# Performance work log

Hardware: AMD Instinct MI355X
Metric: run time of the kernel (lower is better)

## Reference

```python
import jax, jax.numpy as jnp
import numpy as np

NUM, B, C, H, W = 2, 8, 512, 32, 32


def setup_inputs() -> dict:
    key = jax.random.key(0)
    ks = jax.random.split(key, 6)
    s = 0.02  # weight init scale
    return {
        "feat_sources": jax.random.normal(ks[0], (NUM, B, C, H, W), jnp.float32),
        "feat_targets": jax.random.normal(ks[1], (NUM, B, C, H, W), jnp.float32),
        # 1x1 conv == per-pixel channel matmul: weight [num, C_out, C_in], bias [num, C]
        "Wq": jax.random.normal(ks[2], (NUM, C, C), jnp.float32) * s,
        "bq": jnp.zeros((NUM, C), jnp.float32),
        "Wk": jax.random.normal(ks[3], (NUM, C, C), jnp.float32) * s,
        "bk": jnp.zeros((NUM, C), jnp.float32),
        "Wv": jax.random.normal(ks[4], (NUM, C, C), jnp.float32) * s,
        "bv": jnp.zeros((NUM, C), jnp.float32),
    }


def reference(feat_sources, feat_targets, Wq, bq, Wk, bk, Wv, bv):
    num, Bt, Ct, Ht, Wt = feat_targets.shape
    HW = Ht * Wt
    tgt = feat_targets.reshape(num, Bt, Ct, HW)  # queries/values come from targets
    src = feat_sources.reshape(num, Bt, Ct, HW)  # keys come from sources

    # 1x1 conv projections (batched over the `num` heads of convs)
    Q = jnp.einsum('ioc,ibcn->ibno', Wq, tgt) + bq[:, None, None, :]   # (num, B, HW, C)
    K = jnp.einsum('joc,jbcn->jbon', Wk, src) + bk[:, None, :, None]   # (num, B, C, HW)
    V = jnp.einsum('ioc,ibcn->ibon', Wv, tgt) + bv[:, None, :, None]   # (num, B, C, HW)

    # energy[i, j] = bmm(pro_query_i, pro_key_j) over all target/source pairs
    energy = jnp.einsum('ibnc,jbcm->ijbnm', Q, K)                      # (num, num, B, HW, HW)

    # alpha: softmax over sources j of the scalar mean energy per (i, j)
    means = energy.mean(axis=(2, 3, 4))                                # (num, num)
    alphas = jax.nn.softmax(means, axis=1)

    # per-source softmax over keys, then summed across sources (torch.stack(...).sum(0))
    attn = jax.nn.softmax(energy, axis=-1).sum(axis=1)                 # (num, B, HW, HW)

    # out[b, c, n] = sum_m V[b, c, m] * attn[b, n, m]  (bmm(value, attention^T))
    out = jnp.einsum('ibcm,ibnm->ibcn', V, attn).reshape(num, Bt, Ct, Ht, Wt)
    return out, alphas
```

## Files before the change

kernel.cpp:

```cpp
#include <hip/hip_runtime.h>

#define NUMH 2
#define BATCH 8
#define CCH 512
#define HWN 1024

typedef unsigned short u16;
typedef unsigned int u32;
typedef _Float16 f16;
typedef __attribute__((ext_vector_type(8))) _Float16 f16x8;
typedef __attribute__((ext_vector_type(8))) short bf16x8;
typedef __attribute__((ext_vector_type(4))) float f32x4;

__device__ __forceinline__ u16 f2h(float x) {
    union { f16 h; u16 u; } cv;
    cv.h = (f16)x;
    return cv.u;
}
__device__ __forceinline__ u16 f2bf(float x) {
    u32 u = __float_as_uint(x);
    return (u16)((u + 0x7fffu + ((u >> 16) & 1u)) >> 16);
}

__device__ __forceinline__ float waveReduceSum(float v) {
#pragma unroll
    for (int off = 32; off > 0; off >>= 1) v += __shfl_xor(v, off);
    return v;
}

__device__ __forceinline__ void swz_decode(int& x, int& y, int& z) {
    const int gx = gridDim.x, gy = gridDim.y;
    const int nwg = gx * gy * gridDim.z;
    const int fid = blockIdx.x + gx * (blockIdx.y + gy * blockIdx.z);
    const int cpx = nwg >> 3;
    int swz = (fid & 7) * cpx + (fid >> 3);
    x = swz % gx; swz /= gx;
    y = swz % gy; z = swz / gy;
}

__global__ void zero_means_kernel(float* means) {
    if (threadIdx.x < 4) means[threadIdx.x] = 0.0f;
}

__global__ __launch_bounds__(256) void reduce_rs_kernel(const float* __restrict__ rs,
                                                        float* __restrict__ ls, int n) {
    const int idx = blockIdx.x * 256 + threadIdx.x;
    if (idx >= n) return;
    const int slice = idx >> 10, col = idx & 1023;
    const float* p = rs + ((size_t)slice * 16) * HWN + col;
    float s = 0.0f;
#pragma unroll
    for (int k = 0; k < 16; k++) s += p[k * HWN];
    ls[idx] = s;
}

__device__ __forceinline__ void stage_tile(const u16* __restrict__ src, int ld, int k0,
                                           u16* lds_arr, int w, int l) {
#pragma unroll
    for (int inst = 0; inst < 2; inst++) {
        const int p = w * 128 + inst * 64 + l;
        const int n = p >> 2;
        const int k4 = (p & 3) ^ ((n >> 1) & 3);
        const u16* g = src + n * ld + k0 + k4 * 8;
        u16* lp = lds_arr + (w * 128 + inst * 64) * 8;
        __builtin_amdgcn_global_load_lds(
            (const __attribute__((address_space(1))) u32*)g,
            (__attribute__((address_space(3))) u32*)lp, 16, 0, 0);
    }
}

template<bool BF>
__device__ __forceinline__ void mfma_block(const u16* sA, const u16* sB,
                                           int wr, int wc, int fr, int kq, f32x4 acc[4][4]) {
#define SLOT(row) (((row) * 4 + ((kq) ^ (((row) >> 1) & 3))) * 8)
    if constexpr (BF) {
        bf16x8 a[4], b[4];
#pragma unroll
        for (int mi = 0; mi < 4; mi++) a[mi] = *(const bf16x8*)(sA + SLOT(wr * 64 + mi * 16 + fr));
#pragma unroll
        for (int ni = 0; ni < 4; ni++) b[ni] = *(const bf16x8*)(sB + SLOT(wc * 64 + ni * 16 + fr));
#pragma unroll
        for (int mi = 0; mi < 4; mi++)
#pragma unroll
            for (int ni = 0; ni < 4; ni++)
                acc[mi][ni] = __builtin_amdgcn_mfma_f32_16x16x32_bf16(a[mi], b[ni], acc[mi][ni], 0, 0, 0);
    } else {
        f16x8 a[4], b[4];
#pragma unroll
        for (int mi = 0; mi < 4; mi++) a[mi] = *(const f16x8*)(sA + SLOT(wr * 64 + mi * 16 + fr));
#pragma unroll
        for (int ni = 0; ni < 4; ni++) b[ni] = *(const f16x8*)(sB + SLOT(wc * 64 + ni * 16 + fr));
#pragma unroll
        for (int mi = 0; mi < 4; mi++)
#pragma unroll
            for (int ni = 0; ni < 4; ni++)
                acc[mi][ni] = __builtin_amdgcn_mfma_f32_16x16x32_f16(a[mi], b[ni], acc[mi][ni], 0, 0, 0);
    }
#undef SLOT
}

template<bool BF>
__device__ __forceinline__ void mm_core(const u16* __restrict__ A, const u16* __restrict__ B,
                                        int K, int ldA, int ldB, u16* s, f32x4 acc[4][4]) {
    const int t = threadIdx.x, w = t >> 6, l = t & 63;
    const int wr = w >> 1, wc = w & 1, fr = l & 15, kq = l >> 4;
    u16 *sA0 = s, *sA1 = s + 4096, *sB0 = s + 8192, *sB1 = s + 12288;
    for (int k0 = 0; k0 < K; k0 += 64) {
        __syncthreads();
        stage_tile(A, ldA, k0, sA0, w, l);
        stage_tile(A, ldA, k0 + 32, sA1, w, l);
        stage_tile(B, ldB, k0, sB0, w, l);
        stage_tile(B, ldB, k0 + 32, sB1, w, l);
        __syncthreads();
        mfma_block<BF>(sA0, sB0, wr, wc, fr, kq, acc);
        mfma_block<BF>(sA1, sB1, wr, wc, fr, kq, acc);
    }
}

#define ACC_INIT(acc)                                         \
    f32x4 acc[4][4];                                          \
    _Pragma("unroll") for (int mi_ = 0; mi_ < 4; mi_++)       \
    _Pragma("unroll") for (int ni_ = 0; ni_ < 4; ni_++)       \
        acc[mi_][ni_] = (f32x4){0.f, 0.f, 0.f, 0.f};

#define SMEM_BYTES 32768

template<bool BF, bool BCOL, bool BROW>
__device__ __forceinline__ void epi_h16(char* smem, const f32x4 acc[4][4],
                                        const float* biasCol, const float* biasRow,
                                        u16* O, int ldO) {
    const int t = threadIdx.x, w = t >> 6, l = t & 63;
    const int wr = w >> 1, wc = w & 1, fr = l & 15, fq = l >> 4;
    u16* sb16 = (u16*)smem;
    u32* sb32 = (u32*)smem;
#pragma unroll
    for (int half = 0; half < 2; half++) {
        __syncthreads();
        if (wr == half) {
#pragma unroll
            for (int ni = 0; ni < 4; ni++) {
                const int col = wc * 64 + ni * 16 + fr;
                const float bc = BCOL ? biasCol[col] : 0.0f;
#pragma unroll
                for (int mi = 0; mi < 4; mi++)
#pragma unroll
                    for (int r = 0; r < 4; r++) {
                        const int lrow = mi * 16 + fq * 4 + r;
                        const float v = acc[mi][ni][r] + bc +
                                        (BROW ? biasRow[half * 64 + lrow] : 0.0f);
                        sb16[lrow * 132 + col] = BF ? f2bf(v) : f2h(v);
                    }
            }
        }
        __syncthreads();
#pragma unroll
        for (int it = 0; it < 4; it++) {
            const int idx = it * 256 + t;
            const int rr = idx >> 4, ch = idx & 15;
            const uint4 v4 = *(const uint4*)&sb32[rr * 66 + ch * 4];
            *(uint4*)&O[(size_t)(half * 64 + rr) * ldO + ch * 8] = v4;
        }
    }
}

template<bool SCALE>
__device__ __forceinline__ void epi_f32(char* smem, const f32x4 acc[4][4],
                                        const float* ls, float* O, int ldO) {
    const int t = threadIdx.x, w = t >> 6, l = t & 63;
    const int wr = w >> 1, wc = w & 1, fr = l & 15, fq = l >> 4;
    float* sf = (float*)smem;
#pragma unroll
    for (int q = 0; q < 4; q++) {
        __syncthreads();
        if (wr == (q >> 1)) {
            const int mi0 = (q & 1) * 2;
#pragma unroll
            for (int ni = 0; ni < 4; ni++) {
                const int col = wc * 64 + ni * 16 + fr;
                const float inv = SCALE ? 1.0f / ls[col] : 1.0f;
#pragma unroll
                for (int mm = 0; mm < 2; mm++)
#pragma unroll
                    for (int r = 0; r < 4; r++) {
                        const int lrow = mm * 16 + fq * 4 + r;
                        sf[lrow * 132 + col] = acc[mi0 + mm][ni][r] * inv;
                    }
            }
        }
        __syncthreads();
#pragma unroll
        for (int it = 0; it < 4; it++) {
            const int idx = it * 256 + t;
            const int rr = idx >> 5, ch = idx & 31;
            const float4 v4 = *(const float4*)&sf[rr * 132 + ch * 4];
            *(float4*)&O[(size_t)(q * 32 + rr) * ldO + ch * 4] = v4;
        }
    }
}

__global__ __launch_bounds__(256) void tconv_kernel(
    const float* __restrict__ tgt, const float* __restrict__ src,
    u16* __restrict__ Tt, u16* __restrict__ St) {
    __shared__ float s[64][65];
    const int z = blockIdx.z;
    const int ib = z & 15;
    const float* X = (z >> 4 ? src : tgt) + (size_t)ib * CCH * HWN;
    u16* O = (z >> 4 ? St : Tt) + (size_t)ib * HWN * CCH;
    const int n0 = blockIdx.x * 64, c0 = blockIdx.y * 64;
    const int t = threadIdx.x;
    {
        const int cc = t >> 4, nch = (t & 15) * 4;
#pragma unroll
        for (int r = 0; r < 4; r++) {
            const float4 v = *(const float4*)&X[(size_t)(c0 + cc + r * 16) * HWN + n0 + nch];
            s[cc + r * 16][nch + 0] = v.x;
            s[cc + r * 16][nch + 1] = v.y;
            s[cc + r * 16][nch + 2] = v.z;
            s[cc + r * 16][nch + 3] = v.w;
        }
    }
    __syncthreads();
    const int nl = t >> 2;
    const int cb = (t & 3) * 16;
    __attribute__((aligned(16))) u16 hbuf[16];
#pragma unroll
    for (int cc = 0; cc < 16; cc++) hbuf[cc] = f2h(s[cb + cc][nl]);
    const size_t orow = (size_t)(n0 + nl) * CCH + c0 + cb;
    *(uint4*)&O[orow + 0] = *(const uint4*)&hbuf[0];
    *(uint4*)&O[orow + 8] = *(const uint4*)&hbuf[8];
}

__global__ __launch_bounds__(256) void convw_kernel(
    const float* __restrict__ Wq, const float* __restrict__ Wk, const float* __restrict__ Wv,
    u16* __restrict__ Wqh, u16* __restrict__ Wkh, u16* __restrict__ Wvh) {
    const int idx = (blockIdx.x * 256 + threadIdx.x) * 4;
    {
        const float4 v = *(const float4*)&Wq[idx];
        uint2 h = {(u32)f2h(v.x) | ((u32)f2h(v.y) << 16), (u32)f2h(v.z) | ((u32)f2h(v.w) << 16)};
        *(uint2*)&Wqh[idx] = h;
    }
    {
        const float4 v = *(const float4*)&Wk[idx];
        uint2 h = {(u32)f2h(v.x) | ((u32)f2h(v.y) << 16), (u32)f2h(v.z) | ((u32)f2h(v.w) << 16)};
        *(uint2*)&Wkh[idx] = h;
    }
    {
        const float4 v = *(const float4*)&Wv[idx];
        uint2 h = {(u32)f2h(v.x) | ((u32)f2h(v.y) << 16), (u32)f2h(v.z) | ((u32)f2h(v.w) << 16)};
        *(uint2*)&Wvh[idx] = h;
    }
}

__global__ __launch_bounds__(256) void proj_qk_kernel(
    const u16* __restrict__ Tt, const u16* __restrict__ St,
    const u16* __restrict__ Wqh, const u16* __restrict__ Wkh,
    const float* __restrict__ bq, const float* __restrict__ bk,
    u16* __restrict__ Qp, u16* __restrict__ Kp) {
    __shared__ __align__(16) char smem[SMEM_BYTES];
    int bx, by, z;
    swz_decode(bx, by, z);
    const int b = z & 7, i = (z >> 3) & 1, p = z >> 4;
    const size_t ib = (size_t)(i * BATCH + b) * HWN * CCH;
    const u16* A = (p ? St : Tt) + ib;
    const u16* B = (p ? Wkh : Wqh) + (size_t)i * CCH * CCH;
    const float* bias = (p ? bk : bq) + i * CCH;
    u16* O = (p ? Kp : Qp) + ib;
    const int tile_m = by * 128, tile_n = bx * 128;

    ACC_INIT(acc)
    mm_core<false>(A + (size_t)tile_m * CCH, B + (size_t)tile_n * CCH,
                   CCH, CCH, CCH, (u16*)smem, acc);

    epi_h16<false, true, false>(smem, acc, bias + tile_n, nullptr,
                                O + (size_t)tile_m * CCH + tile_n, CCH);
}

__global__ __launch_bounds__(256) void proj_v_kernel(
    const u16* __restrict__ Wvh, const u16* __restrict__ Tt,
    const float* __restrict__ bvv, u16* __restrict__ Vb) {
    __shared__ __align__(16) char smem[SMEM_BYTES];
    int bx, by, z;
    swz_decode(bx, by, z);
    const int b = z & 7, i = z >> 3;
    const size_t ib = (size_t)(i * BATCH + b) * HWN * CCH;
    const u16* A = Wvh + (size_t)i * CCH * CCH;
    const u16* B = Tt + ib;
    const int tile_m = by * 128, tile_n = bx * 128;

    ACC_INIT(acc)
    mm_core<false>(A + (size_t)tile_m * CCH, B + (size_t)tile_n * CCH,
                   CCH, CCH, CCH, (u16*)smem, acc);

    u16* Ov = Vb + (size_t)(i * BATCH + b) * CCH * HWN;
    epi_h16<true, false, true>(smem, acc, nullptr, bvv + i * CCH + tile_m,
                               Ov + (size_t)tile_m * HWN + tile_n, HWN);
}

__global__ __launch_bounds__(256) void gemmE_kernel(
    const u16* __restrict__ Qp, const u16* __restrict__ Kp,
    u16* __restrict__ P, float* __restrict__ rs, float* __restrict__ means,
    int b0, int Bc) {
    __shared__ __align__(16) char smem[33792];
    __shared__ float redsum[4];
    int bx, by, z;
    swz_decode(bx, by, z);
    const int j = z & 1, ib2 = z >> 1;
    const int i = ib2 / Bc, bb = ib2 % Bc, b = b0 + bb;
    const size_t offA = (size_t)(i * BATCH + b) * HWN * CCH;
    const size_t offB = (size_t)(j * BATCH + b) * HWN * CCH;
    const int tile_m = by * 128, tile_n = bx * 128;
    u16* Po = P + (size_t)(ib2 * 2 + j) * HWN * HWN + (size_t)tile_m * HWN + tile_n;

    ACC_INIT(acc)
    mm_core<false>(Qp + offA + (size_t)tile_m * CCH, Kp + offB + (size_t)tile_n * CCH,
                   CCH, CCH, CCH, (u16*)smem, acc);

    const int t = threadIdx.x, w = t >> 6, l = t & 63;
    const int wr = w >> 1, wc = w & 1, fr = l & 15, fq = l >> 4;
    u16* sb16 = (u16*)smem;
    u32* sb32 = (u32*)smem;
    float* rsp = rs + ((size_t)(ib2 * 2 + j) * 16 + (bx * 2 + wc)) * HWN;
    __syncthreads();
    float tsum = 0.0f;
    float rowacc[4][4];
#pragma unroll
    for (int mi = 0; mi < 4; mi++)
#pragma unroll
        for (int r = 0; r < 4; r++) rowacc[mi][r] = 0.0f;
#pragma unroll
    for (int ni = 0; ni < 4; ni++) {
        const int col = wc * 64 + ni * 16 + fr;
#pragma unroll
        for (int mi = 0; mi < 4; mi++)
#pragma unroll
            for (int r = 0; r < 4; r++) {
                const int row = wr * 64 + mi * 16 + fq * 4 + r;
                const float raw = acc[mi][ni][r];
                tsum += raw;
                const float ex = __expf(raw);
                rowacc[mi][r] += ex;
                sb16[row * 132 + col] = f2bf(ex);
            }
    }
    tsum = waveReduceSum(tsum);
    if (l == 0) redsum[w] = tsum;
#pragma unroll
    for (int mi = 0; mi < 4; mi++)
#pragma unroll
        for (int r = 0; r < 4; r++) {
            float v = rowacc[mi][r];
            v += __shfl_xor(v, 1); v += __shfl_xor(v, 2);
            v += __shfl_xor(v, 4); v += __shfl_xor(v, 8);
            if (fr == 0) rsp[tile_m + wr * 64 + mi * 16 + fq * 4 + r] = v;
        }
    __syncthreads();
    if (t == 0) atomicAdd(&means[i * 2 + j], redsum[0] + redsum[1] + redsum[2] + redsum[3]);
#pragma unroll
    for (int it = 0; it < 8; it++) {
        const int idx = it * 256 + t;
        const int rr = idx >> 4, ch = idx & 15;
        const uint4 v4 = *(const uint4*)&sb32[rr * 66 + ch * 4];
        *(uint4*)&Po[(size_t)rr * HWN + ch * 8] = v4;
    }
}

__global__ __launch_bounds__(256) void gemmOut_kernel(
    const u16* __restrict__ Vb, const u16* __restrict__ P, const float* __restrict__ ls,
    float* __restrict__ outp, int b0, int Bc) {
    __shared__ __align__(16) char smem[SMEM_BYTES];
    int bx, by, ib2;
    swz_decode(bx, by, ib2);
    const int i = ib2 / Bc, bb = ib2 % Bc, b = b0 + bb;
    const u16* A = Vb + (size_t)(i * BATCH + b) * CCH * HWN;
    const u16* P0 = P + (size_t)(ib2 * 2 + 0) * HWN * HWN;
    const u16* P1 = P + (size_t)(ib2 * 2 + 1) * HWN * HWN;
    const float* ls0 = ls + (size_t)(ib2 * 2 + 0) * HWN;
    const float* ls1 = ls + (size_t)(ib2 * 2 + 1) * HWN;
    float* O = outp + (size_t)(i * BATCH + b) * CCH * HWN;
    const int tile_m = by * 128, tile_n = bx * 128;
    const int t = threadIdx.x, w = t >> 6, l = t & 63;
    const int wc = w & 1, fr = l & 15;

    ACC_INIT(acc)
    mm_core<true>(A + (size_t)tile_m * HWN, P0 + (size_t)tile_n * HWN,
                  HWN, HWN, HWN, (u16*)smem, acc);
#pragma unroll
    for (int ni = 0; ni < 4; ni++) {
        const int col = tile_n + wc * 64 + ni * 16 + fr;
        const float sc = ls1[col] / ls0[col];
#pragma unroll
        for (int mi = 0; mi < 4; mi++) acc[mi][ni] *= sc;
    }
    mm_core<true>(A + (size_t)tile_m * HWN, P1 + (size_t)tile_n * HWN,
                  HWN, HWN, HWN, (u16*)smem, acc);

    epi_f32<true>(smem, acc, ls1 + tile_n, O + (size_t)tile_m * HWN + tile_n, HWN);
}

__global__ void alphas_kernel(const float* __restrict__ means, float* __restrict__ outp) {
    if (threadIdx.x != 0) return;
    const float cnt = (float)BATCH * (float)HWN * (float)HWN;
    float m[4];
#pragma unroll
    for (int k = 0; k < 4; k++) m[k] = means[k] / cnt;
#pragma unroll
    for (int i = 0; i < 2; i++) {
        const float a = m[i * 2 + 0], bsc = m[i * 2 + 1];
        const float mx = fmaxf(a, bsc);
        const float ea = __expf(a - mx), eb = __expf(bsc - mx);
        const float inv = 1.0f / (ea + eb);
        outp[i * 2 + 0] = ea * inv;
        outp[i * 2 + 1] = eb * inv;
    }
}

extern "C" void kernel_launch(void* const* d_in, const int* in_sizes, int n_in,
                              void* d_out, int out_size, void* d_ws, size_t ws_size,
                              hipStream_t stream) {
    const float* fsrc = (const float*)d_in[0];
    const float* ftgt = (const float*)d_in[1];
    const float* Wq = (const float*)d_in[2];
    const float* bq = (const float*)d_in[3];
    const float* Wk = (const float*)d_in[4];
    const float* bk = (const float*)d_in[5];
    const float* Wv = (const float*)d_in[6];
    const float* bv = (const float*)d_in[7];
    float* outp = (float*)d_out;

    const size_t SZ_ACT = (size_t)NUMH * BATCH * HWN * CCH * 2;
    const size_t SZ_W = (size_t)NUMH * CCH * CCH * 2;
    char* w = (char*)d_ws;
    u16* Qp = (u16*)w; w += SZ_ACT;
    u16* Kp = (u16*)w; w += SZ_ACT;
    u16* Vb = (u16*)w; w += SZ_ACT;
    u16* Wqh = (u16*)w; w += SZ_W;
    u16* Wkh = (u16*)w; w += SZ_W;
    u16* Wvh = (u16*)w; w += SZ_W;
    float* means = (float*)w; w += 64;
    float* rs = (float*)w; w += (size_t)NUMH * BATCH * 2 * 16 * HWN * 4;
    float* ls = (float*)w; w += (size_t)NUMH * BATCH * 2 * HWN * 4;
    char* region = w;
    u16* Tt = (u16*)region;
    u16* St = (u16*)(region + SZ_ACT);

    const size_t base_used = (size_t)(region - (char*)d_ws);
    int Bc = 8;
    while (Bc > 1) {
        size_t need = (size_t)NUMH * Bc * 2 * HWN * HWN * 2;
        size_t tneed = need > 2 * SZ_ACT ? need : 2 * SZ_ACT;
        if (base_used + tneed <= ws_size) break;
        Bc >>= 1;
    }
    u16* P = (u16*)region;

    zero_means_kernel<<<1, 64, 0, stream>>>(means);
    convw_kernel<<<512, 256, 0, stream>>>(Wq, Wk, Wv, Wqh, Wkh, Wvh);
    tconv_kernel<<<dim3(16, 8, 32), 256, 0, stream>>>(ftgt, fsrc, Tt, St);
    proj_qk_kernel<<<dim3(4, 8, 32), 256, 0, stream>>>(Tt, St, Wqh, Wkh, bq, bk, Qp, Kp);
    proj_v_kernel<<<dim3(8, 4, 16), 256, 0, stream>>>(Wvh, Tt, bv, Vb);

    const int nch = BATCH / Bc;
    for (int ch = 0; ch < nch; ch++) {
        const int b0 = ch * Bc;
        const int nls = NUMH * Bc * 2 * HWN;
        gemmE_kernel<<<dim3(8, 8, NUMH * Bc * 2), 256, 0, stream>>>(Qp, Kp, P, rs, means, b0, Bc);
        reduce_rs_kernel<<<(nls + 255) / 256, 256, 0, stream>>>(rs, ls, nls);
        gemmOut_kernel<<<dim3(8, 4, NUMH * Bc), 256, 0, stream>>>(Vb, P, ls, outp, b0, Bc);
    }
    alphas_kernel<<<1, 1, 0, stream>>>(means, outp + (out_size - 4));
}
```

Measured before the change: 189.8 us.

## Double-buffer energy GEMM staging and fold log2e into Q weights for exp2

Adds a double-buffered GEMM main loop for the energy kernel so the next K-slice is staged into shared memory while MFMAs run on the current one. Q weights and bias are prescaled by log2(e) so the softmax exponent becomes a native exp2f, and the mean is rescaled by ln2 in the alpha kernel. The P tile store is moved ahead of the row-sum reductions. The prescaling adds some fp16 rounding error in Q, and the energy GEMM now needs extra synchronisation.

```diff
diff --git a/kernel.cpp b/kernel.cpp
--- a/kernel.cpp
+++ b/kernel.cpp
@@ -4,6 +4,8 @@
 #define BATCH 8
 #define CCH 512
 #define HWN 1024
+#define LOG2E 1.4426950408889634f
+#define LN2F 0.6931471805599453f
 
 typedef unsigned short u16;
 typedef unsigned int u32;
@@ -117,6 +119,28 @@
     }
 }
 
+__device__ __forceinline__ void mm_core_db(const u16* __restrict__ A, const u16* __restrict__ B,
+                                           int K, int ldA, int ldB, u16* s, f32x4 acc[4][4]) {
+    const int t = threadIdx.x, w = t >> 6, l = t & 63;
+    const int wr = w >> 1, wc = w & 1, fr = l & 15, kq = l >> 4;
+    u16 *sA0 = s, *sB0 = s + 4096, *sA1 = s + 8192, *sB1 = s + 12288;
+    stage_tile(A, ldA, 0, sA0, w, l);
+    stage_tile(B, ldB, 0, sB0, w, l);
+    __syncthreads();
+    for (int k0 = 0; k0 < K; k0 += 64) {
+        stage_tile(A, ldA, k0 + 32, sA1, w, l);
+        stage_tile(B, ldB, k0 + 32, sB1, w, l);
+        mfma_block<false>(sA0, sB0, wr, wc, fr, kq, acc);
+        __syncthreads();
+        if (k0 + 64 < K) {
+            stage_tile(A, ldA, k0 + 64, sA0, w, l);
+            stage_tile(B, ldB, k0 + 64, sB0, w, l);
+        }
+        mfma_block<false>(sA1, sB1, wr, wc, fr, kq, acc);
+        __syncthreads();
+    }
+}
+
 #define ACC_INIT(acc)                                         \
     f32x4 acc[4][4];                                          \
     _Pragma("unroll") for (int mi_ = 0; mi_ < 4; mi_++)       \
@@ -127,7 +151,8 @@
 
 template<bool BF, bool BCOL, bool BROW>
 __device__ __forceinline__ void epi_h16(char* smem, const f32x4 acc[4][4],
-                                        const float* biasCol, const float* biasRow,
+                                        const float* biasCol, float bcScale,
+                                        const float* biasRow,
                                         u16* O, int ldO) {
     const int t = threadIdx.x, w = t >> 6, l = t & 63;
     const int wr = w >> 1, wc = w & 1, fr = l & 15, fq = l >> 4;
@@ -140,7 +165,7 @@
 #pragma unroll
             for (int ni = 0; ni < 4; ni++) {
                 const int col = wc * 64 + ni * 16 + fr;
-                const float bc = BCOL ? biasCol[col] : 0.0f;
+                const float bc = BCOL ? biasCol[col] * bcScale : 0.0f;
 #pragma unroll
                 for (int mi = 0; mi < 4; mi++)
 #pragma unroll
@@ -236,7 +261,8 @@
     const int idx = (blockIdx.x * 256 + threadIdx.x) * 4;
     {
         const float4 v = *(const float4*)&Wq[idx];
-        uint2 h = {(u32)f2h(v.x) | ((u32)f2h(v.y) << 16), (u32)f2h(v.z) | ((u32)f2h(v.w) << 16)};
+        uint2 h = {(u32)f2h(v.x * LOG2E) | ((u32)f2h(v.y * LOG2E) << 16),
+                   (u32)f2h(v.z * LOG2E) | ((u32)f2h(v.w * LOG2E) << 16)};
         *(uint2*)&Wqh[idx] = h;
     }
     {
@@ -271,7 +297,7 @@
     mm_core<false>(A + (size_t)tile_m * CCH, B + (size_t)tile_n * CCH,
                    CCH, CCH, CCH, (u16*)smem, acc);
 
-    epi_h16<false, true, false>(smem, acc, bias + tile_n, nullptr,
+    epi_h16<false, true, false>(smem, acc, bias + tile_n, p ? 1.0f : LOG2E, nullptr,
                                 O + (size_t)tile_m * CCH + tile_n, CCH);
 }
 
@@ -292,7 +318,7 @@
                    CCH, CCH, CCH, (u16*)smem, acc);
 
     u16* Ov = Vb + (size_t)(i * BATCH + b) * CCH * HWN;
-    epi_h16<true, false, true>(smem, acc, nullptr, bvv + i * CCH + tile_m,
+    epi_h16<true, false, true>(smem, acc, nullptr, 1.0f, bvv + i * CCH + tile_m,
                                Ov + (size_t)tile_m * HWN + tile_n, HWN);
 }
 
@@ -312,15 +338,14 @@
     u16* Po = P + (size_t)(ib2 * 2 + j) * HWN * HWN + (size_t)tile_m * HWN + tile_n;
 
     ACC_INIT(acc)
-    mm_core<false>(Qp + offA + (size_t)tile_m * CCH, Kp + offB + (size_t)tile_n * CCH,
-                   CCH, CCH, CCH, (u16*)smem, acc);
+    mm_core_db(Qp + offA + (size_t)tile_m * CCH, Kp + offB + (size_t)tile_n * CCH,
+               CCH, CCH, CCH, (u16*)smem, acc);
 
     const int t = threadIdx.x, w = t >> 6, l = t & 63;
     const int wr = w >> 1, wc = w & 1, fr = l & 15, fq = l >> 4;
     u16* sb16 = (u16*)smem;
     u32* sb32 = (u32*)smem;
     float* rsp = rs + ((size_t)(ib2 * 2 + j) * 16 + (bx * 2 + wc)) * HWN;
-    __syncthreads();
     float tsum = 0.0f;
     float rowacc[4][4];
 #pragma unroll
@@ -337,10 +362,18 @@
                 const int row = wr * 64 + mi * 16 + fq * 4 + r;
                 const float raw = acc[mi][ni][r];
                 tsum += raw;
-                const float ex = __expf(raw);
+                const float ex = exp2f(raw);
                 rowacc[mi][r] += ex;
                 sb16[row * 132 + col] = f2bf(ex);
             }
+    }
+    __syncthreads();
+#pragma unroll
+    for (int it = 0; it < 8; it++) {
+        const int idx = it * 256 + t;
+        const int rr = idx >> 4, ch = idx & 15;
+        const uint4 v4 = *(const uint4*)&sb32[rr * 66 + ch * 4];
+        *(uint4*)&Po[(size_t)rr * HWN + ch * 8] = v4;
     }
     tsum = waveReduceSum(tsum);
     if (l == 0) redsum[w] = tsum;
@@ -355,13 +388,6 @@
         }
     __syncthreads();
     if (t == 0) atomicAdd(&means[i * 2 + j], redsum[0] + redsum[1] + redsum[2] + redsum[3]);
-#pragma unroll
-    for (int it = 0; it < 8; it++) {
-        const int idx = it * 256 + t;
-        const int rr = idx >> 4, ch = idx & 15;
-        const uint4 v4 = *(const uint4*)&sb32[rr * 66 + ch * 4];
-        *(uint4*)&Po[(size_t)rr * HWN + ch * 8] = v4;
-    }
 }
 
 __global__ __launch_bounds__(256) void gemmOut_kernel(
@@ -402,7 +428,7 @@
     const float cnt = (float)BATCH * (float)HWN * (float)HWN;
     float m[4];
 #pragma unroll
-    for (int k = 0; k < 4; k++) m[k] = means[k] / cnt;
+    for (int k = 0; k < 4; k++) m[k] = means[k] / cnt * LN2F;
 #pragma unroll
     for (int i = 0; i < 2; i++) {
         const float a = m[i * 2 + 0], bsc = m[i * 2 + 1];
```

Measured after the change: 202.2 us. 6.5% more time.
